# Kernel optimization log

Measured on AMD Instinct MI355X. Metric: run time of the kernel, lower is better.

Reference implementation:

```python
import jax, jax.numpy as jnp
import numpy as np

# Grouped masked GEMM dims (see DeepSeekMOE._up_gate/_down):
# G = num_experts // ep = 8; M = m_per_group = 32
# up/gate: k = hidden_size = 4096, n = 2*expert_dim = 2816
# down   : k = expert_dim  = 1408, n = hidden_size = 4096
G, M = 8, 32
K_UG, N_UG = 4096, 2816
K_DN, N_DN = 1408, 4096


def setup_inputs() -> dict:
    key = jax.random.key(0)
    k1, k2, k3, k4, k5 = jax.random.split(key, 5)
    x_ug = jax.random.normal(k1, (G, M, K_UG), dtype=jnp.float32)
    w_ug = jax.random.normal(k2, (G, N_UG, K_UG), dtype=jnp.float32) * 0.02  # NT layout [g, n, k]
    x_dn = jax.random.normal(k3, (G, M, K_DN), dtype=jnp.float32)
    w_dn = jax.random.normal(k4, (G, N_DN, K_DN), dtype=jnp.float32) * 0.02  # NT layout [g, n, k]
    masked_m = jax.random.randint(k5, (G,), 0, M, dtype=jnp.int32)  # per-group valid row count
    return {"x_ug": x_ug, "w_ug": w_ug, "x_dn": x_dn, "w_dn": w_dn, "masked_m": masked_m}


def reference(x_ug, w_ug, x_dn, w_dn, masked_m):
    # Row-validity mask: rows >= masked_m[g] are skipped by the masked grouped GEMM
    # (their output is zero / undefined; we define it as zero).
    row = jnp.arange(M, dtype=jnp.int32)
    mask = (row[None, :] < masked_m[:, None])[:, :, None]  # [G, M, 1]

    # Masked grouped GEMM, NT layout: out[g] = x[g] @ w[g].T on valid rows.
    out_ug = jnp.einsum('gmk,gnk->gmn', x_ug, w_ug)  # [G, M, N_UG]  up/gate proj
    out_dn = jnp.einsum('gmk,gnk->gmn', x_dn, w_dn)  # [G, M, N_DN]  down proj

    out_ug = jnp.where(mask, out_ug, jnp.zeros((), out_ug.dtype))
    out_dn = jnp.where(mask, out_dn, jnp.zeros((), out_dn.dtype))
    # Pack both grouped-GEMM outputs into one array along the feature dim.
    return jnp.concatenate([out_ug, out_dn], axis=-1)  # [G, M, N_UG + N_DN]
```

## Files before the change

### kernel.cpp

```cpp
#include <hip/hip_runtime.h>
#include <hip/hip_bf16.h>


#define G_    8
#define M_    32
#define KUG   4096
#define NUG   2816
#define KDN   1408
#define NDN   4096
#define NOUT  (NUG + NDN)
#define BN    32
#define BK    128
#define UPT   (NUG / BN)
#define DNT   (NDN / BN)
#define UPG   (UPT + DNT)
#define XUG_E (G_ * M_ * KUG)
#define XDN_E (G_ * M_ * KDN)
#define XBF_BYTES ((size_t)(XUG_E + XDN_E) * 2)

typedef __attribute__((ext_vector_type(8))) short bf16x8;
typedef __attribute__((ext_vector_type(4))) float f32x4;

typedef __attribute__((address_space(3))) float        lds_f32;
typedef const __attribute__((address_space(1))) float  gbl_f32;

#define SCHED0() __builtin_amdgcn_sched_barrier(0)

__device__ __forceinline__ short f2bf(float x) {
  union { __hip_bfloat16 h; short s; } u;
  u.h = __hip_bfloat16(x);
  return u.s;
}

__device__ __forceinline__ bf16x8 cvt8(f32x4 lo, f32x4 hi) {
  bf16x8 o;
#pragma unroll
  for (int j = 0; j < 4; ++j) { o[j] = f2bf(lo[j]); o[4 + j] = f2bf(hi[j]); }
  return o;
}

__global__ void cvt_x_kernel(const float* __restrict__ src, short* __restrict__ dst,
                             int n8) {
  int i = blockIdx.x * 256 + threadIdx.x;
  if (i < n8) {
    f32x4 lo = *(const f32x4*)(src + (size_t)i * 8);
    f32x4 hi = *(const f32x4*)(src + (size_t)i * 8 + 4);
    *(bf16x8*)(dst + (size_t)i * 8) = cvt8(lo, hi);
  }
}

__device__ __forceinline__ void stageW(const float* wg, float* wbuf, int K,
                                       int k0, int t) {
#pragma unroll
  for (int i = 0; i < 16; ++i) {
    int gid = i * 64 + t;
    int row = gid >> 5;
    int q   = gid & 31;
    int qs  = q ^ (row & 7);
    __builtin_amdgcn_global_load_lds(
        (gbl_f32*)(wg + (size_t)row * K + k0 + qs * 4),
        (lds_f32*)(wbuf + gid * 4), 16, 0, 0);
  }
}

__device__ __forceinline__ void loadX(const short* xq, int K, int k0, int r,
                                      int q4, bf16x8 (&xb)[2][4]) {
#pragma unroll
  for (int mf = 0; mf < 2; ++mf)
#pragma unroll
    for (int ks = 0; ks < 4; ++ks)
      xb[mf][ks] = *(const bf16x8*)(xq + (size_t)(mf * 16 + r) * K +
                                    k0 + ks * 32 + q4 * 8);
}

__device__ __forceinline__ void readW(const float* wbuf, int r, int q4, int sk,
                                      f32x4 (&wr)[2][4][2]) {
#pragma unroll
  for (int nf = 0; nf < 2; ++nf) {
    const float* rowp = wbuf + (size_t)(nf * 16 + r) * BK;
#pragma unroll
    for (int ks = 0; ks < 4; ++ks) {
      int g0 = (ks * 4 + q4) * 2;
      wr[nf][ks][0] = *(const f32x4*)(rowp + (((g0)     ^ sk) << 2));
      wr[nf][ks][1] = *(const f32x4*)(rowp + (((g0 + 1) ^ sk) << 2));
    }
  }
}

__device__ __forceinline__ void mfma_iter(const f32x4 (&wr)[2][4][2],
                                          const bf16x8 (&xb)[2][4],
                                          f32x4 (&acc)[2][2]) {
#pragma unroll
  for (int ks = 0; ks < 4; ++ks) {
    bf16x8 b0 = cvt8(wr[0][ks][0], wr[0][ks][1]);
    bf16x8 b1 = cvt8(wr[1][ks][0], wr[1][ks][1]);
    acc[0][0] = __builtin_amdgcn_mfma_f32_16x16x32_bf16(xb[0][ks], b0, acc[0][0], 0, 0, 0);
    acc[1][0] = __builtin_amdgcn_mfma_f32_16x16x32_bf16(xb[1][ks], b0, acc[1][0], 0, 0, 0);
    acc[0][1] = __builtin_amdgcn_mfma_f32_16x16x32_bf16(xb[0][ks], b1, acc[0][1], 0, 0, 0);
    acc[1][1] = __builtin_amdgcn_mfma_f32_16x16x32_bf16(xb[1][ks], b1, acc[1][1], 0, 0, 0);
  }
}

template<int NIT>
__device__ __forceinline__ void run_unit(const float* wg, const short* xq, int K,
                                         float* wbuf, int t, f32x4 (&acc)[2][2]) {
  int r = t & 15, q4 = t >> 4, sk = r & 7;
  bf16x8 xA[2][4], xB[2][4];

  stageW(wg, wbuf, K, 0, t);  SCHED0();
  loadX(xq, K, 0, r, q4, xA); SCHED0();

  constexpr int NP = NIT / 2;
  for (int p = 0; p < NP; ++p) {
    int itA = 2 * p, itB = itA + 1;
    asm volatile("s_waitcnt vmcnt(8)" ::: "memory");  SCHED0();
    f32x4 wr[2][4][2];
    readW(wbuf, r, q4, sk, wr);                       SCHED0();
    stageW(wg, wbuf, K, itB * BK, t);                 SCHED0();
    loadX(xq, K, itB * BK, r, q4, xB);                SCHED0();
    mfma_iter(wr, xA, acc);
    asm volatile("s_waitcnt vmcnt(8)" ::: "memory");  SCHED0();
    readW(wbuf, r, q4, sk, wr);                       SCHED0();
    if (itB + 1 < NIT) {
      stageW(wg, wbuf, K, (itB + 1) * BK, t);         SCHED0();
      loadX(xq, K, (itB + 1) * BK, r, q4, xA);        SCHED0();
    }
    mfma_iter(wr, xB, acc);
  }
  if constexpr (NIT & 1) {
    asm volatile("s_waitcnt vmcnt(8)" ::: "memory");  SCHED0();
    f32x4 wr[2][4][2];
    readW(wbuf, r, q4, sk, wr);                       SCHED0();
    mfma_iter(wr, xA, acc);
  }
}

__global__ __launch_bounds__(64, 2) void moe_masked_gemm(
    const float* __restrict__ w_ug, const float* __restrict__ w_dn,
    const short* __restrict__ xbf_ug, const short* __restrict__ xbf_dn,
    const int* __restrict__ masked_m, float* __restrict__ out) {
  __shared__ float wbuf[BN * BK];

  int b = blockIdx.x;
  int g = b & 7;
  int u = b >> 3;

  const float* wg;
  const short* xq;
  int K, n0, colOff;
  bool is_up = (u < UPT);
  if (is_up) {
    K = KUG; n0 = u * BN; colOff = 0;
    wg = w_ug + ((size_t)g * NUG + n0) * KUG;
    xq = xbf_ug + (size_t)g * M_ * KUG;
  } else {
    int d = u - UPT;
    K = KDN; n0 = d * BN; colOff = NUG;
    wg = w_dn + ((size_t)g * NDN + n0) * KDN;
    xq = xbf_dn + (size_t)g * M_ * KDN;
  }

  int mm = masked_m[g];
  int t  = threadIdx.x;
  int r  = t & 15, q4 = t >> 4;

  f32x4 acc[2][2];
#pragma unroll
  for (int mf = 0; mf < 2; ++mf)
#pragma unroll
    for (int nf = 0; nf < 2; ++nf) acc[mf][nf] = (f32x4){0.f, 0.f, 0.f, 0.f};

  if (mm != 0) {
    if (is_up) run_unit<KUG / BK>(wg, xq, K, wbuf, t, acc);
    else       run_unit<KDN / BK>(wg, xq, K, wbuf, t, acc);
  }

  float* outg = out + (size_t)g * M_ * NOUT + colOff + n0;
#pragma unroll
  for (int i = 0; i < 4; ++i) {
    int m0 = q4 * 4 + i, m1 = 16 + m0;
    bool v0 = m0 < mm, v1 = m1 < mm;
#pragma unroll
    for (int nf = 0; nf < 2; ++nf) {
      outg[(size_t)m0 * NOUT + nf * 16 + r] = v0 ? acc[0][nf][i] : 0.f;
      outg[(size_t)m1 * NOUT + nf * 16 + r] = v1 ? acc[1][nf][i] : 0.f;
    }
  }
}

__global__ __launch_bounds__(64, 2) void moe_masked_gemm_f32(
    const float* __restrict__ x_ug, const float* __restrict__ w_ug,
    const float* __restrict__ x_dn, const float* __restrict__ w_dn,
    const int* __restrict__ masked_m, float* __restrict__ out) {
  __shared__ float wbuf[BN * BK];
  int b = blockIdx.x, g = b & 7, u = b >> 3;
  const float* wg; const float* xf;
  int K, n0, colOff, NIT;
  bool is_up = (u < UPT);
  if (is_up) { K = KUG; NIT = KUG / BK; n0 = u * BN; colOff = 0;
    wg = w_ug + ((size_t)g * NUG + n0) * KUG; xf = x_ug + (size_t)g * M_ * KUG;
  } else { int d = u - UPT; K = KDN; NIT = KDN / BK; n0 = d * BN; colOff = NUG;
    wg = w_dn + ((size_t)g * NDN + n0) * KDN; xf = x_dn + (size_t)g * M_ * KDN; }
  int mm = masked_m[g], t = threadIdx.x, r = t & 15, q4 = t >> 4, sk = r & 7;
  f32x4 acc[2][2];
#pragma unroll
  for (int mf = 0; mf < 2; ++mf)
#pragma unroll
    for (int nf = 0; nf < 2; ++nf) acc[mf][nf] = (f32x4){0.f, 0.f, 0.f, 0.f};
  if (mm != 0) {
    for (int it = 0; it < NIT; ++it) {
      int k0 = it * BK;
      stageW(wg, wbuf, K, k0, t);
      bf16x8 xb[2][4];
#pragma unroll
      for (int mf = 0; mf < 2; ++mf)
#pragma unroll
        for (int ks = 0; ks < 4; ++ks) {
          const float* xp = xf + (size_t)(mf * 16 + r) * K + k0 + ks * 32 + q4 * 8;
          xb[mf][ks] = cvt8(*(const f32x4*)xp, *(const f32x4*)(xp + 4));
        }
      asm volatile("s_waitcnt vmcnt(0)" ::: "memory");
      SCHED0();
      f32x4 wr[2][4][2];
      readW(wbuf, r, q4, sk, wr);
      mfma_iter(wr, xb, acc);
    }
  }
  float* outg = out + (size_t)g * M_ * NOUT + colOff + n0;
#pragma unroll
  for (int i = 0; i < 4; ++i) {
    int m0 = q4 * 4 + i, m1 = 16 + m0;
    bool v0 = m0 < mm, v1 = m1 < mm;
#pragma unroll
    for (int nf = 0; nf < 2; ++nf) {
      outg[(size_t)m0 * NOUT + nf * 16 + r] = v0 ? acc[0][nf][i] : 0.f;
      outg[(size_t)m1 * NOUT + nf * 16 + r] = v1 ? acc[1][nf][i] : 0.f;
    }
  }
}

extern "C" void kernel_launch(void* const* d_in, const int* in_sizes, int n_in,
                              void* d_out, int out_size, void* d_ws, size_t ws_size,
                              hipStream_t stream) {
  const float* x_ug     = (const float*)d_in[0];
  const float* w_ug     = (const float*)d_in[1];
  const float* x_dn     = (const float*)d_in[2];
  const float* w_dn     = (const float*)d_in[3];
  const int*   masked_m = (const int*)d_in[4];
  float*       out      = (float*)d_out;

  short* xbf_ug = (short*)d_ws;
  short* xbf_dn = xbf_ug + XUG_E;

  if (ws_size >= XBF_BYTES) {
    cvt_x_kernel<<<dim3(XUG_E / 8 / 256), dim3(256), 0, stream>>>(x_ug, xbf_ug, XUG_E / 8);
    cvt_x_kernel<<<dim3(XDN_E / 8 / 256), dim3(256), 0, stream>>>(x_dn, xbf_dn, XDN_E / 8);
    moe_masked_gemm<<<dim3(G_ * UPG), dim3(64), 0, stream>>>(
        w_ug, w_dn, xbf_ug, xbf_dn, masked_m, out);
  } else {
    moe_masked_gemm_f32<<<dim3(G_ * UPG), dim3(64), 0, stream>>>(
        x_ug, w_ug, x_dn, w_dn, masked_m, out);
  }
}
```

Before: 132.0 us.

## Restructure up-proj pipeline with 16-row half tiles, interleave block order, fuse cvt launches

```diff
diff --git a/kernel.cpp b/kernel.cpp
--- a/kernel.cpp
+++ b/kernel.cpp
@@ -10,7 +10,6 @@
 #define NDN   4096
 #define NOUT  (NUG + NDN)
 #define BN    32
-#define BK    128
 #define UPT   (NUG / BN)
 #define DNT   (NDN / BN)
 #define UPG   (UPT + DNT)
@@ -25,13 +24,14 @@
 typedef const __attribute__((address_space(1))) float  gbl_f32;
 
 #define SCHED0() __builtin_amdgcn_sched_barrier(0)
+#define VMC0()   asm volatile("s_waitcnt vmcnt(0)" ::: "memory")
+#define VMC16()  asm volatile("s_waitcnt vmcnt(16)" ::: "memory")
 
 __device__ __forceinline__ short f2bf(float x) {
   union { __hip_bfloat16 h; short s; } u;
   u.h = __hip_bfloat16(x);
   return u.s;
 }
-
 __device__ __forceinline__ bf16x8 cvt8(f32x4 lo, f32x4 hi) {
   bf16x8 o;
 #pragma unroll
@@ -39,18 +39,79 @@
   return o;
 }
 
-__global__ void cvt_x_kernel(const float* __restrict__ src, short* __restrict__ dst,
-                             int n8) {
+__global__ void cvt_x_kernel(const float* __restrict__ xu, const float* __restrict__ xd,
+                             short* __restrict__ du, short* __restrict__ dd) {
   int i = blockIdx.x * 256 + threadIdx.x;
-  if (i < n8) {
-    f32x4 lo = *(const f32x4*)(src + (size_t)i * 8);
-    f32x4 hi = *(const f32x4*)(src + (size_t)i * 8 + 4);
-    *(bf16x8*)(dst + (size_t)i * 8) = cvt8(lo, hi);
-  }
-}
-
-__device__ __forceinline__ void stageW(const float* wg, float* wbuf, int K,
-                                       int k0, int t) {
+  const float* s; short* d;
+  int j = i;
+  if (i < XUG_E / 8) { s = xu; d = du; }
+  else { s = xd; d = dd; j = i - XUG_E / 8; if (j >= XDN_E / 8) return; }
+  f32x4 lo = *(const f32x4*)(s + (size_t)j * 8);
+  f32x4 hi = *(const f32x4*)(s + (size_t)j * 8 + 4);
+  *(bf16x8*)(d + (size_t)j * 8) = cvt8(lo, hi);
+}
+
+__device__ __forceinline__ void stage16_1k(const float* wrows, float* wbuf,
+                                           int k0, int t) {
+#pragma unroll
+  for (int i = 0; i < 16; ++i) {
+    int qs = t ^ (i & 7);
+    __builtin_amdgcn_global_load_lds(
+        (gbl_f32*)(wrows + (size_t)i * KUG + k0 + qs * 4),
+        (lds_f32*)(wbuf + i * 256 + t * 4), 16, 0, 0);
+  }
+}
+__device__ __forceinline__ void readW8(const float* wbuf, int r, int q4, int sk,
+                                       f32x4 (&wr)[8][2]) {
+  const float* rowp = wbuf + (size_t)r * 256;
+#pragma unroll
+  for (int ks = 0; ks < 8; ++ks) {
+    int g0 = ks * 8 + q4 * 2;
+    wr[ks][0] = *(const f32x4*)(rowp + (((g0)     ^ sk) << 2));
+    wr[ks][1] = *(const f32x4*)(rowp + (((g0 + 1) ^ sk) << 2));
+  }
+}
+__device__ __forceinline__ void loadX16(const short* xq, int k0, int r, int q4,
+                                        bf16x8 (&xb)[2][8]) {
+#pragma unroll
+  for (int mf = 0; mf < 2; ++mf)
+#pragma unroll
+    for (int ks = 0; ks < 8; ++ks)
+      xb[mf][ks] = *(const bf16x8*)(xq + (size_t)(mf * 16 + r) * KUG +
+                                    k0 + ks * 32 + q4 * 8);
+}
+__device__ __forceinline__ void mfma8(const f32x4 (&wr)[8][2], const bf16x8 (&xb)[2][8],
+                                      f32x4& aA, f32x4& aB) {
+#pragma unroll
+  for (int ks = 0; ks < 8; ++ks) {
+    bf16x8 bb = cvt8(wr[ks][0], wr[ks][1]);
+    aA = __builtin_amdgcn_mfma_f32_16x16x32_bf16(xb[0][ks], bb, aA, 0, 0, 0);
+    aB = __builtin_amdgcn_mfma_f32_16x16x32_bf16(xb[1][ks], bb, aB, 0, 0, 0);
+  }
+}
+
+template<bool LAST>
+__device__ __forceinline__ void up_tile(const float* wg, const short* xq, float* wbuf,
+                                        int j, int t, int r, int q4, int sk,
+                                        bf16x8 (&XC)[2][8], bf16x8 (&XN)[2][8],
+                                        f32x4 (&acc)[2][2]) {
+  int k0 = j * 256;
+  VMC0(); SCHED0();
+  f32x4 wr0[8][2];
+  readW8(wbuf, r, q4, sk, wr0); SCHED0();
+  stage16_1k(wg + (size_t)16 * KUG, wbuf, k0, t);
+  SCHED0();
+  if (!LAST) { loadX16(xq, k0 + 256, r, q4, XN); SCHED0(); }
+  mfma8(wr0, XC, acc[0][0], acc[1][0]);
+  if (!LAST) { VMC16(); } else { VMC0(); }
+  SCHED0();
+  f32x4 wr1[8][2];
+  readW8(wbuf, r, q4, sk, wr1); SCHED0();
+  if (!LAST) { stage16_1k(wg, wbuf, k0 + 256, t); SCHED0(); }
+  mfma8(wr1, XC, acc[0][1], acc[1][1]);
+}
+
+__device__ __forceinline__ void stageW32(const float* wg, float* wbuf, int k0, int t) {
 #pragma unroll
   for (int i = 0; i < 16; ++i) {
     int gid = i * 64 + t;
@@ -58,80 +119,8 @@
     int q   = gid & 31;
     int qs  = q ^ (row & 7);
     __builtin_amdgcn_global_load_lds(
-        (gbl_f32*)(wg + (size_t)row * K + k0 + qs * 4),
+        (gbl_f32*)(wg + (size_t)row * KDN + k0 + qs * 4),
         (lds_f32*)(wbuf + gid * 4), 16, 0, 0);
-  }
-}
-
-__device__ __forceinline__ void loadX(const short* xq, int K, int k0, int r,
-                                      int q4, bf16x8 (&xb)[2][4]) {
-#pragma unroll
-  for (int mf = 0; mf < 2; ++mf)
-#pragma unroll
-    for (int ks = 0; ks < 4; ++ks)
-      xb[mf][ks] = *(const bf16x8*)(xq + (size_t)(mf * 16 + r) * K +
-                                    k0 + ks * 32 + q4 * 8);
-}
-
-__device__ __forceinline__ void readW(const float* wbuf, int r, int q4, int sk,
-                                      f32x4 (&wr)[2][4][2]) {
-#pragma unroll
-  for (int nf = 0; nf < 2; ++nf) {
-    const float* rowp = wbuf + (size_t)(nf * 16 + r) * BK;
-#pragma unroll
-    for (int ks = 0; ks < 4; ++ks) {
-      int g0 = (ks * 4 + q4) * 2;
-      wr[nf][ks][0] = *(const f32x4*)(rowp + (((g0)     ^ sk) << 2));
-      wr[nf][ks][1] = *(const f32x4*)(rowp + (((g0 + 1) ^ sk) << 2));
-    }
-  }
-}
-
-__device__ __forceinline__ void mfma_iter(const f32x4 (&wr)[2][4][2],
-                                          const bf16x8 (&xb)[2][4],
-                                          f32x4 (&acc)[2][2]) {
-#pragma unroll
-  for (int ks = 0; ks < 4; ++ks) {
-    bf16x8 b0 = cvt8(wr[0][ks][0], wr[0][ks][1]);
-    bf16x8 b1 = cvt8(wr[1][ks][0], wr[1][ks][1]);
-    acc[0][0] = __builtin_amdgcn_mfma_f32_16x16x32_bf16(xb[0][ks], b0, acc[0][0], 0, 0, 0);
-    acc[1][0] = __builtin_amdgcn_mfma_f32_16x16x32_bf16(xb[1][ks], b0, acc[1][0], 0, 0, 0);
-    acc[0][1] = __builtin_amdgcn_mfma_f32_16x16x32_bf16(xb[0][ks], b1, acc[0][1], 0, 0, 0);
-    acc[1][1] = __builtin_amdgcn_mfma_f32_16x16x32_bf16(xb[1][ks], b1, acc[1][1], 0, 0, 0);
-  }
-}
-
-template<int NIT>
-__device__ __forceinline__ void run_unit(const float* wg, const short* xq, int K,
-                                         float* wbuf, int t, f32x4 (&acc)[2][2]) {
-  int r = t & 15, q4 = t >> 4, sk = r & 7;
-  bf16x8 xA[2][4], xB[2][4];
-
-  stageW(wg, wbuf, K, 0, t);  SCHED0();
-  loadX(xq, K, 0, r, q4, xA); SCHED0();
-
-  constexpr int NP = NIT / 2;
-  for (int p = 0; p < NP; ++p) {
-    int itA = 2 * p, itB = itA + 1;
-    asm volatile("s_waitcnt vmcnt(8)" ::: "memory");  SCHED0();
-    f32x4 wr[2][4][2];
-    readW(wbuf, r, q4, sk, wr);                       SCHED0();
-    stageW(wg, wbuf, K, itB * BK, t);                 SCHED0();
-    loadX(xq, K, itB * BK, r, q4, xB);                SCHED0();
-    mfma_iter(wr, xA, acc);
-    asm volatile("s_waitcnt vmcnt(8)" ::: "memory");  SCHED0();
-    readW(wbuf, r, q4, sk, wr);                       SCHED0();
-    if (itB + 1 < NIT) {
-      stageW(wg, wbuf, K, (itB + 1) * BK, t);         SCHED0();
-      loadX(xq, K, (itB + 1) * BK, r, q4, xA);        SCHED0();
-    }
-    mfma_iter(wr, xB, acc);
-  }
-  if constexpr (NIT & 1) {
-    asm volatile("s_waitcnt vmcnt(8)" ::: "memory");  SCHED0();
-    f32x4 wr[2][4][2];
-    readW(wbuf, r, q4, sk, wr);                       SCHED0();
-    mfma_iter(wr, xA, acc);
   }
 }
 
@@ -139,30 +128,18 @@
     const float* __restrict__ w_ug, const float* __restrict__ w_dn,
     const short* __restrict__ xbf_ug, const short* __restrict__ xbf_dn,
     const int* __restrict__ masked_m, float* __restrict__ out) {
-  __shared__ float wbuf[BN * BK];
+  __shared__ float wbuf[4096];
 
   int b = blockIdx.x;
   int g = b & 7;
-  int u = b >> 3;
-
-  const float* wg;
-  const short* xq;
-  int K, n0, colOff;
-  bool is_up = (u < UPT);
-  if (is_up) {
-    K = KUG; n0 = u * BN; colOff = 0;
-    wg = w_ug + ((size_t)g * NUG + n0) * KUG;
-    xq = xbf_ug + (size_t)g * M_ * KUG;
-  } else {
-    int d = u - UPT;
-    K = KDN; n0 = d * BN; colOff = NUG;
-    wg = w_dn + ((size_t)g * NDN + n0) * KDN;
-    xq = xbf_dn + (size_t)g * M_ * KDN;
-  }
+  int v = b >> 3;
+  int p = v / 27, s = v - p * 27;
+  int ub = (s * 11 + 16) / 27;
+  bool is_up = ((s * 11) % 27) < 11;
 
   int mm = masked_m[g];
   int t  = threadIdx.x;
-  int r  = t & 15, q4 = t >> 4;
+  int r  = t & 15, q4 = t >> 4, sk = r & 7;
 
   f32x4 acc[2][2];
 #pragma unroll
@@ -170,9 +147,55 @@
 #pragma unroll
     for (int nf = 0; nf < 2; ++nf) acc[mf][nf] = (f32x4){0.f, 0.f, 0.f, 0.f};
 
-  if (mm != 0) {
-    if (is_up) run_unit<KUG / BK>(wg, xq, K, wbuf, t, acc);
-    else       run_unit<KDN / BK>(wg, xq, K, wbuf, t, acc);
+  int n0, colOff;
+  if (is_up) {
+    int u = p * 11 + ub;
+    n0 = u * BN; colOff = 0;
+    const float* wg = w_ug + ((size_t)g * NUG + n0) * KUG;
+    const short* xq = xbf_ug + (size_t)g * M_ * KUG;
+    if (mm != 0) {
+      constexpr int NT = KUG / 256;
+      bf16x8 xA[2][8], xB[2][8];
+      stage16_1k(wg, wbuf, 0, t); SCHED0();
+      loadX16(xq, 0, r, q4, xA);  SCHED0();
+      for (int pp = 0; pp < NT / 2 - 1; ++pp) {
+        up_tile<false>(wg, xq, wbuf, 2 * pp,     t, r, q4, sk, xA, xB, acc);
+        up_tile<false>(wg, xq, wbuf, 2 * pp + 1, t, r, q4, sk, xB, xA, acc);
+      }
+      up_tile<false>(wg, xq, wbuf, NT - 2, t, r, q4, sk, xA, xB, acc);
+      up_tile<true >(wg, xq, wbuf, NT - 1, t, r, q4, sk, xB, xA, acc);
+    }
+  } else {
+    int d = p * 16 + (s - ub);
+    n0 = d * BN; colOff = NUG;
+    const float* wg = w_dn + ((size_t)g * NDN + n0) * KDN;
+    const short* xq = xbf_dn + (size_t)g * M_ * KDN;
+    if (mm != 0) {
+      for (int it = 0; it < KDN / 128; ++it) {
+        int k0 = it * 128;
+        stageW32(wg, wbuf, k0, t);
+        bf16x8 xb[2][4];
+#pragma unroll
+        for (int mf = 0; mf < 2; ++mf)
+#pragma unroll
+          for (int ks = 0; ks < 4; ++ks)
+            xb[mf][ks] = *(const bf16x8*)(xq + (size_t)(mf * 16 + r) * KDN +
+                                          k0 + ks * 32 + q4 * 8);
+        VMC0(); SCHED0();
+#pragma unroll
+        for (int ks = 0; ks < 4; ++ks) {
+          int g0 = (ks * 4 + q4) * 2;
+          int o0 = ((g0 ^ sk) << 2), o1 = (((g0 + 1) ^ sk) << 2);
+#pragma unroll
+          for (int nf = 0; nf < 2; ++nf) {
+            const float* rowp = wbuf + (size_t)(nf * 16 + r) * 128;
+            bf16x8 bb = cvt8(*(const f32x4*)(rowp + o0), *(const f32x4*)(rowp + o1));
+            acc[0][nf] = __builtin_amdgcn_mfma_f32_16x16x32_bf16(xb[0][ks], bb, acc[0][nf], 0, 0, 0);
+            acc[1][nf] = __builtin_amdgcn_mfma_f32_16x16x32_bf16(xb[1][ks], bb, acc[1][nf], 0, 0, 0);
+          }
+        }
+      }
+    }
   }
 
   float* outg = out + (size_t)g * M_ * NOUT + colOff + n0;
@@ -192,14 +215,14 @@
     const float* __restrict__ x_ug, const float* __restrict__ w_ug,
     const float* __restrict__ x_dn, const float* __restrict__ w_dn,
     const int* __restrict__ masked_m, float* __restrict__ out) {
-  __shared__ float wbuf[BN * BK];
+  __shared__ float wbuf[4096];
   int b = blockIdx.x, g = b & 7, u = b >> 3;
   const float* wg; const float* xf;
   int K, n0, colOff, NIT;
   bool is_up = (u < UPT);
-  if (is_up) { K = KUG; NIT = KUG / BK; n0 = u * BN; colOff = 0;
+  if (is_up) { K = KUG; NIT = 32; n0 = u * BN; colOff = 0;
     wg = w_ug + ((size_t)g * NUG + n0) * KUG; xf = x_ug + (size_t)g * M_ * KUG;
-  } else { int d = u - UPT; K = KDN; NIT = KDN / BK; n0 = d * BN; colOff = NUG;
+  } else { int d = u - UPT; K = KDN; NIT = 11; n0 = d * BN; colOff = NUG;
     wg = w_dn + ((size_t)g * NDN + n0) * KDN; xf = x_dn + (size_t)g * M_ * KDN; }
   int mm = masked_m[g], t = threadIdx.x, r = t & 15, q4 = t >> 4, sk = r & 7;
   f32x4 acc[2][2];
@@ -209,8 +232,13 @@
     for (int nf = 0; nf < 2; ++nf) acc[mf][nf] = (f32x4){0.f, 0.f, 0.f, 0.f};
   if (mm != 0) {
     for (int it = 0; it < NIT; ++it) {
-      int k0 = it * BK;
-      stageW(wg, wbuf, K, k0, t);
+      int k0 = it * 128;
+#pragma unroll
+      for (int i = 0; i < 16; ++i) {
+        int gid = i * 64 + t, row = gid >> 5, q = gid & 31, qs = q ^ (row & 7);
+        __builtin_amdgcn_global_load_lds((gbl_f32*)(wg + (size_t)row * K + k0 + qs * 4),
+                                         (lds_f32*)(wbuf + gid * 4), 16, 0, 0);
+      }
       bf16x8 xb[2][4];
 #pragma unroll
       for (int mf = 0; mf < 2; ++mf)
@@ -219,11 +247,19 @@
           const float* xp = xf + (size_t)(mf * 16 + r) * K + k0 + ks * 32 + q4 * 8;
           xb[mf][ks] = cvt8(*(const f32x4*)xp, *(const f32x4*)(xp + 4));
         }
-      asm volatile("s_waitcnt vmcnt(0)" ::: "memory");
-      SCHED0();
-      f32x4 wr[2][4][2];
-      readW(wbuf, r, q4, sk, wr);
-      mfma_iter(wr, xb, acc);
+      VMC0(); SCHED0();
+#pragma unroll
+      for (int ks = 0; ks < 4; ++ks) {
+        int g0 = (ks * 4 + q4) * 2;
+        int o0 = ((g0 ^ sk) << 2), o1 = (((g0 + 1) ^ sk) << 2);
+#pragma unroll
+        for (int nf = 0; nf < 2; ++nf) {
+          const float* rowp = wbuf + (size_t)(nf * 16 + r) * 128;
+          bf16x8 bb = cvt8(*(const f32x4*)(rowp + o0), *(const f32x4*)(rowp + o1));
+          acc[0][nf] = __builtin_amdgcn_mfma_f32_16x16x32_bf16(xb[0][ks], bb, acc[0][nf], 0, 0, 0);
+          acc[1][nf] = __builtin_amdgcn_mfma_f32_16x16x32_bf16(xb[1][ks], bb, acc[1][nf], 0, 0, 0);
+        }
+      }
     }
   }
   float* outg = out + (size_t)g * M_ * NOUT + colOff + n0;
@@ -253,8 +289,9 @@
   short* xbf_dn = xbf_ug + XUG_E;
 
   if (ws_size >= XBF_BYTES) {
-    cvt_x_kernel<<<dim3(XUG_E / 8 / 256), dim3(256), 0, stream>>>(x_ug, xbf_ug, XUG_E / 8);
-    cvt_x_kernel<<<dim3(XDN_E / 8 / 256), dim3(256), 0, stream>>>(x_dn, xbf_dn, XDN_E / 8);
+    int n8 = (XUG_E + XDN_E) / 8;
+    cvt_x_kernel<<<dim3((n8 + 255) / 256), dim3(256), 0, stream>>>(
+        x_ug, x_dn, xbf_ug, xbf_dn);
     moe_masked_gemm<<<dim3(G_ * UPG), dim3(64), 0, stream>>>(
         w_ug, w_dn, xbf_ug, xbf_dn, masked_m, out);
   } else {
```

After: 152.2 us. 1.15x slower.
